# Performance work log

Measured on AMD Instinct MI355X. Metric: run time of the kernel, lower is better.

The kernel has to match this reference:

```python
import jax, jax.numpy as jnp
import numpy as np

N_NODES = 20000
N_EDGES = 200000
N_TOK = 8          # N patch tokens per node
IN_DIM = 64        # C
N_HEADS = 4
HEAD_DIM = 16      # out_dim


def setup_inputs() -> dict:
    key = jax.random.key(0)
    ks = jax.random.split(key, 16)
    scale = 1.0 / np.sqrt(IN_DIM).astype(np.float32)
    def lin(i):
        W = jax.random.normal(ks[i], (IN_DIM, N_HEADS * HEAD_DIM), dtype=jnp.float32) * scale
        b = jax.random.normal(ks[i + 1], (N_HEADS * HEAD_DIM,), dtype=jnp.float32) * 0.01
        return W, b
    Qw, Qb = lin(0)
    Kw, Kb = lin(2)
    Vw, Vb = lin(4)
    Ew, Eb = lin(6)
    h = jax.random.normal(ks[8], (N_NODES, N_TOK, IN_DIM), dtype=jnp.float32)
    e = jax.random.normal(ks[9], (N_EDGES, N_TOK, IN_DIM), dtype=jnp.float32)
    src = jax.random.randint(ks[10], (N_EDGES,), 0, N_NODES)
    dst = jax.random.randint(ks[11], (N_EDGES,), 0, N_NODES)
    return {"h": h, "e": e, "src": src, "dst": dst,
            "Qw": Qw, "Qb": Qb, "Kw": Kw, "Kb": Kb,
            "Vw": Vw, "Vb": Vb, "Ew": Ew, "Eb": Eb}


def _proj(x, W, b):
    # x: [M, N, C] -> [M, N, H, D]
    y = x @ W + b
    return y.reshape(x.shape[0], x.shape[1], N_HEADS, HEAD_DIM)


def reference(h, e, src, dst, Qw, Qb, Kw, Kb, Vw, Vb, Ew, Eb):
    Qh = _proj(h, Qw, Qb)   # [n, N, H, D]
    Kh = _proj(h, Kw, Kb)
    Vh = _proj(h, Vw, Vb)
    pe = _proj(e, Ew, Eb)   # [E, N, H, D]
    inv_sqrt_d = jnp.float32(1.0 / np.sqrt(HEAD_DIM))
    # edge-wise elementwise QK score, scaled, plus relative PE
    score = Kh[src] * Qh[dst] * inv_sqrt_d + pe   # [E, N, H, D]
    e_out = score
    # exp of head-dim-summed clamped score
    s = jnp.exp(jnp.clip(jnp.sum(score, axis=-1, keepdims=True), -5.0, 5.0))  # [E, N, H, 1]
    wV = jax.ops.segment_sum(Vh[src] * s, dst, num_segments=N_NODES)  # [n, N, H, D]
    z = jax.ops.segment_sum(s, dst, num_segments=N_NODES)             # [n, N, H, 1]
    h_out = wV / (z + 1e-6)
    return h_out, e_out
```

## Files before the change

### kernel.cpp

```cpp
#include <hip/hip_runtime.h>
#include <hip/hip_bf16.h>

#define IN_DIM 64
#define N_TOK 8
#define OUT_DIM 64
#define HEAD_DIM 16
#define N_HEADS 4

__global__ void zero_kernel(int* p, int n) {
    int i = blockIdx.x * blockDim.x + threadIdx.x;
    if (i < n) p[i] = 0;
}

__global__ void hist_kernel(const int* __restrict__ dst, int* __restrict__ deg, int n) {
    int i = blockIdx.x * blockDim.x + threadIdx.x;
    if (i < n) atomicAdd(&deg[dst[i]], 1);
}

__global__ void scan_kernel(const int* __restrict__ deg, int* __restrict__ offs,
                            int* __restrict__ cur, int n) {
    __shared__ int wsum[17];
    __shared__ int carry;
    const int tid = threadIdx.x;
    const int lane = tid & 63;
    const int wid = tid >> 6;
    if (tid == 0) carry = 0;
    __syncthreads();
    for (int base = 0; base < n; base += 1024) {
        const int i = base + tid;
        const int v = (i < n) ? deg[i] : 0;
        int x = v;
#pragma unroll
        for (int d = 1; d < 64; d <<= 1) {
            int y = __shfl_up(x, d);
            if (lane >= d) x += y;
        }
        if (lane == 63) wsum[wid] = x;
        __syncthreads();
        if (wid == 0 && lane < 16) {
            const int a = wsum[lane];
            int s = a;
#pragma unroll
            for (int d = 1; d < 16; d <<= 1) {
                int y = __shfl_up(s, d);
                if (lane >= d) s += y;
            }
            wsum[lane] = s - a;
            if (lane == 15) wsum[16] = s;
        }
        __syncthreads();
        const int excl = x - v + wsum[wid] + carry;
        if (i < n) { offs[i] = excl; cur[i] = excl; }
        __syncthreads();
        if (tid == 0) carry += wsum[16];
        __syncthreads();
    }
    if (tid == 0) offs[n] = carry;
}

__global__ void scatter_kernel(const int* __restrict__ dst, int* __restrict__ cur,
                               int* __restrict__ csr, int n) {
    int i = blockIdx.x * blockDim.x + threadIdx.x;
    if (i < n) {
        int pos = atomicAdd(&cur[dst[i]], 1);
        csr[pos] = i;
    }
}

__device__ __forceinline__ void proj16_acc(const float* __restrict__ tile, int lane,
                                           const float* __restrict__ wb,
                                           float acc[16]) {
#pragma unroll 8
    for (int k = 0; k < 64; ++k) {
        const float ev = tile[lane * 65 + k];
        const float4 w0 = *reinterpret_cast<const float4*>(wb + k * 64);
        const float4 w1 = *reinterpret_cast<const float4*>(wb + k * 64 + 4);
        const float4 w2 = *reinterpret_cast<const float4*>(wb + k * 64 + 8);
        const float4 w3 = *reinterpret_cast<const float4*>(wb + k * 64 + 12);
        acc[0]  = fmaf(ev, w0.x, acc[0]);
        acc[1]  = fmaf(ev, w0.y, acc[1]);
        acc[2]  = fmaf(ev, w0.z, acc[2]);
        acc[3]  = fmaf(ev, w0.w, acc[3]);
        acc[4]  = fmaf(ev, w1.x, acc[4]);
        acc[5]  = fmaf(ev, w1.y, acc[5]);
        acc[6]  = fmaf(ev, w1.z, acc[6]);
        acc[7]  = fmaf(ev, w1.w, acc[7]);
        acc[8]  = fmaf(ev, w2.x, acc[8]);
        acc[9]  = fmaf(ev, w2.y, acc[9]);
        acc[10] = fmaf(ev, w2.z, acc[10]);
        acc[11] = fmaf(ev, w2.w, acc[11]);
        acc[12] = fmaf(ev, w3.x, acc[12]);
        acc[13] = fmaf(ev, w3.y, acc[13]);
        acc[14] = fmaf(ev, w3.z, acc[14]);
        acc[15] = fmaf(ev, w3.w, acc[15]);
    }
}

__device__ __forceinline__ void init16_bias(const float* __restrict__ bb, float acc[16]) {
    const float4 b0 = *reinterpret_cast<const float4*>(bb);
    const float4 b1 = *reinterpret_cast<const float4*>(bb + 4);
    const float4 b2 = *reinterpret_cast<const float4*>(bb + 8);
    const float4 b3 = *reinterpret_cast<const float4*>(bb + 12);
    acc[0] = b0.x;  acc[1] = b0.y;  acc[2] = b0.z;  acc[3] = b0.w;
    acc[4] = b1.x;  acc[5] = b1.y;  acc[6] = b1.z;  acc[7] = b1.w;
    acc[8] = b2.x;  acc[9] = b2.y;  acc[10] = b2.z; acc[11] = b2.w;
    acc[12] = b3.x; acc[13] = b3.y; acc[14] = b3.z; acc[15] = b3.w;
}

__global__ void __launch_bounds__(256) hproj_kernel(
    const float* __restrict__ h,
    const float* __restrict__ Qw, const float* __restrict__ Qb,
    const float* __restrict__ Kw, const float* __restrict__ Kb,
    const float* __restrict__ Vw, const float* __restrict__ Vb,
    float* __restrict__ Qh, float* __restrict__ Kh, float* __restrict__ Vh,
    int nrows) {
    __shared__ float tile[64 * 65];
    const int t = threadIdx.x;
    const int lane = t & 63;
    const int chunk = __builtin_amdgcn_readfirstlane(t >> 6);
    const int row0 = blockIdx.x * 64;
    if (row0 >= nrows) return;

#pragma unroll
    for (int i = 0; i < 4; ++i) {
        const int f = i * 1024 + t * 4;
        const float4 v = *reinterpret_cast<const float4*>(h + (size_t)row0 * 64 + f);
        const int r = f >> 6, c = f & 63;
        tile[r * 65 + c + 0] = v.x;
        tile[r * 65 + c + 1] = v.y;
        tile[r * 65 + c + 2] = v.z;
        tile[r * 65 + c + 3] = v.w;
    }
    __syncthreads();

    float aq[16], ak[16], av[16];
    init16_bias(Qb + chunk * 16, aq);
    proj16_acc(tile, lane, Qw + chunk * 16, aq);
    init16_bias(Kb + chunk * 16, ak);
    proj16_acc(tile, lane, Kw + chunk * 16, ak);
    init16_bias(Vb + chunk * 16, av);
    proj16_acc(tile, lane, Vw + chunk * 16, av);

    __syncthreads();
#pragma unroll
    for (int j = 0; j < 16; ++j) tile[lane * 65 + chunk * 16 + j] = aq[j] * 0.25f;
    __syncthreads();
#pragma unroll
    for (int i = 0; i < 4; ++i) {
        const int f = i * 1024 + t * 4;
        const int r = f >> 6, c = f & 63;
        *reinterpret_cast<float4*>(Qh + (size_t)row0 * 64 + f) =
            make_float4(tile[r * 65 + c], tile[r * 65 + c + 1],
                        tile[r * 65 + c + 2], tile[r * 65 + c + 3]);
    }
    __syncthreads();
#pragma unroll
    for (int j = 0; j < 16; ++j) tile[lane * 65 + chunk * 16 + j] = ak[j];
    __syncthreads();
#pragma unroll
    for (int i = 0; i < 4; ++i) {
        const int f = i * 1024 + t * 4;
        const int r = f >> 6, c = f & 63;
        *reinterpret_cast<float4*>(Kh + (size_t)row0 * 64 + f) =
            make_float4(tile[r * 65 + c], tile[r * 65 + c + 1],
                        tile[r * 65 + c + 2], tile[r * 65 + c + 3]);
    }
    __syncthreads();
#pragma unroll
    for (int j = 0; j < 16; ++j) tile[lane * 65 + chunk * 16 + j] = av[j];
    __syncthreads();
#pragma unroll
    for (int i = 0; i < 4; ++i) {
        const int f = i * 1024 + t * 4;
        const int r = f >> 6, c = f & 63;
        *reinterpret_cast<float4*>(Vh + (size_t)row0 * 64 + f) =
            make_float4(tile[r * 65 + c], tile[r * 65 + c + 1],
                        tile[r * 65 + c + 2], tile[r * 65 + c + 3]);
    }
}

__global__ void __launch_bounds__(256) edge_kernel(
    const float* __restrict__ e,
    const int* __restrict__ src, const int* __restrict__ dst,
    const float* __restrict__ Ew, const float* __restrict__ Eb,
    const float* __restrict__ Qh, const float* __restrict__ Kh,
    float* __restrict__ e_out, float* __restrict__ s_buf,
    int npairs, int n_edges) {
    __shared__ float et[64 * 65];
    __shared__ float kt[64 * 68];
    __shared__ float qt[64 * 68];
    const int t = threadIdx.x;
    const int lane = t & 63;
    const int chunk = __builtin_amdgcn_readfirstlane(t >> 6);
    const int p0 = blockIdx.x * 64;
    const int e0 = p0 >> 3;
    if (p0 >= npairs) return;

#pragma unroll
    for (int i = 0; i < 4; ++i) {
        const int f = i * 1024 + t * 4;
        const float4 v = *reinterpret_cast<const float4*>(e + (size_t)p0 * 64 + f);
        const int r = f >> 6, c = f & 63;
        et[r * 65 + c + 0] = v.x;
        et[r * 65 + c + 1] = v.y;
        et[r * 65 + c + 2] = v.z;
        et[r * 65 + c + 3] = v.w;
    }

    float4* kt4 = reinterpret_cast<float4*>(kt);
    float4* qt4 = reinterpret_cast<float4*>(qt);
#pragma unroll
    for (int i = 0; i < 4; ++i) {
        const int f = i * 1024 + t * 4;
        int ee = e0 + (f >> 9);
        if (ee >= n_edges) ee = n_edges - 1;
        const int o = f & 511;
        const int se = src[ee];
        const int de = dst[ee];
        const float4 kv = *reinterpret_cast<const float4*>(Kh + (size_t)se * 512 + o);
        const float4 qv = *reinterpret_cast<const float4*>(Qh + (size_t)de * 512 + o);
        const int r = f >> 6, c4 = (f & 63) >> 2;
        kt4[r * 17 + c4] = kv;
        qt4[r * 17 + c4] = qv;
    }
    __syncthreads();

    float acc[16];
    init16_bias(Eb + chunk * 16, acc);
    proj16_acc(et, lane, Ew + chunk * 16, acc);

#pragma unroll
    for (int c4 = 0; c4 < 4; ++c4) {
        const float4 kv = kt4[lane * 17 + chunk * 4 + c4];
        const float4 qv = qt4[lane * 17 + chunk * 4 + c4];
        acc[c4 * 4 + 0] = fmaf(kv.x, qv.x, acc[c4 * 4 + 0]);
        acc[c4 * 4 + 1] = fmaf(kv.y, qv.y, acc[c4 * 4 + 1]);
        acc[c4 * 4 + 2] = fmaf(kv.z, qv.z, acc[c4 * 4 + 2]);
        acc[c4 * 4 + 3] = fmaf(kv.w, qv.w, acc[c4 * 4 + 3]);
    }

    {
        float s01 = (acc[0] + acc[1]) + (acc[2] + acc[3]);
        float s23 = (acc[4] + acc[5]) + (acc[6] + acc[7]);
        float s45 = (acc[8] + acc[9]) + (acc[10] + acc[11]);
        float s67 = (acc[12] + acc[13]) + (acc[14] + acc[15]);
        float ssum = (s01 + s23) + (s45 + s67);
        ssum = fminf(fmaxf(ssum, -5.f), 5.f);
        s_buf[(size_t)chunk * npairs + p0 + lane] = __expf(ssum);
    }

    __syncthreads();
#pragma unroll
    for (int j = 0; j < 16; ++j) et[lane * 65 + chunk * 16 + j] = acc[j];
    __syncthreads();
#pragma unroll
    for (int i = 0; i < 4; ++i) {
        const int f = i * 1024 + t * 4;
        const int r = f >> 6, c = f & 63;
        *reinterpret_cast<float4*>(e_out + (size_t)p0 * 64 + f) =
            make_float4(et[r * 65 + c], et[r * 65 + c + 1],
                        et[r * 65 + c + 2], et[r * 65 + c + 3]);
    }
}

__global__ void __launch_bounds__(256) gather_kernel(
    const float* __restrict__ Vh, const float* __restrict__ s_buf,
    const int* __restrict__ src,
    const int* __restrict__ offs, const int* __restrict__ csr,
    float* __restrict__ h_out, int nunits, int npairs) {
    const int unit = blockIdx.x * 4 + (threadIdx.x >> 6);
    const int lane = threadIdx.x & 63;
    if (unit >= nunits) return;
    const int node = unit >> 3;
    const int tok = unit & 7;
    const int beg = offs[node];
    const int end = offs[node + 1];
    const int hh = lane >> 4;
    const float* sb = s_buf + (size_t)hh * npairs + tok;
    float acc = 0.f;
    float z = 0.f;
    for (int base = beg; base < end; base += 64) {
        const int nn = min(64, end - base);
        int eid = 0, sidx = 0;
        if (lane < nn) {
            eid = csr[base + lane];
            sidx = src[eid];
        }
        int j = 0;
        for (; j + 1 < nn; j += 2) {
            const int ej0 = __shfl(eid, j),     ej1 = __shfl(eid, j + 1);
            const int sj0 = __shfl(sidx, j),    sj1 = __shfl(sidx, j + 1);
            const float sh0 = sb[(size_t)ej0 * 8];
            const float sh1 = sb[(size_t)ej1 * 8];
            const float v0 = Vh[((size_t)sj0 * 8 + tok) * 64 + lane];
            const float v1 = Vh[((size_t)sj1 * 8 + tok) * 64 + lane];
            acc = fmaf(v0, sh0, acc); z += sh0;
            acc = fmaf(v1, sh1, acc); z += sh1;
        }
        if (j < nn) {
            const int ej = __shfl(eid, j);
            const int sj = __shfl(sidx, j);
            const float sh = sb[(size_t)ej * 8];
            const float v = Vh[((size_t)sj * 8 + tok) * 64 + lane];
            acc = fmaf(v, sh, acc); z += sh;
        }
    }
    h_out[(size_t)unit * OUT_DIM + lane] = acc / (z + 1e-6f);
}

extern "C" void kernel_launch(void* const* d_in, const int* in_sizes, int n_in,
                              void* d_out, int out_size, void* d_ws, size_t ws_size,
                              hipStream_t stream) {
    const float* h  = (const float*)d_in[0];
    const float* e  = (const float*)d_in[1];
    const int* src  = (const int*)d_in[2];
    const int* dst  = (const int*)d_in[3];
    const float* Qw = (const float*)d_in[4];
    const float* Qb = (const float*)d_in[5];
    const float* Kw = (const float*)d_in[6];
    const float* Kb = (const float*)d_in[7];
    const float* Vw = (const float*)d_in[8];
    const float* Vb = (const float*)d_in[9];
    const float* Ew = (const float*)d_in[10];
    const float* Eb = (const float*)d_in[11];

    const int n_nodes = in_sizes[0] / (N_TOK * IN_DIM);
    const int n_edges = in_sizes[2];
    const int nrows   = n_nodes * N_TOK;
    const int npairs  = n_edges * N_TOK;
    const int h_out_elems = n_nodes * N_TOK * OUT_DIM;

    float* h_out = (float*)d_out;
    float* e_out = (float*)d_out + h_out_elems;

    float* Qh    = (float*)d_ws;
    float* Kh    = Qh + (size_t)nrows * OUT_DIM;
    float* Vh    = Kh + (size_t)nrows * OUT_DIM;
    float* s_buf = Vh + (size_t)nrows * OUT_DIM;
    int*   deg   = (int*)(s_buf + (size_t)npairs * N_HEADS);
    int*   offs  = deg + n_nodes;
    int*   cur   = offs + (n_nodes + 1);
    int*   csr   = cur + n_nodes;

    zero_kernel<<<(n_nodes + 255) / 256, 256, 0, stream>>>(deg, n_nodes);
    hist_kernel<<<(n_edges + 255) / 256, 256, 0, stream>>>(dst, deg, n_edges);
    scan_kernel<<<1, 1024, 0, stream>>>(deg, offs, cur, n_nodes);
    scatter_kernel<<<(n_edges + 255) / 256, 256, 0, stream>>>(dst, cur, csr, n_edges);

    hproj_kernel<<<(nrows + 63) / 64, 256, 0, stream>>>(
        h, Qw, Qb, Kw, Kb, Vw, Vb, Qh, Kh, Vh, nrows);

    edge_kernel<<<(npairs + 63) / 64, 256, 0, stream>>>(
        e, src, dst, Ew, Eb, Qh, Kh, e_out, s_buf, npairs, n_edges);

    gather_kernel<<<(nrows + 3) / 4, 256, 0, stream>>>(
        Vh, s_buf, src, offs, csr, h_out, nrows, npairs);
}
```

Measured before the change: 990.4 us.

## Store scores pair-major and gather four tokens per wave with float4 loads

The exp scores buffer is now laid out per pair with the heads contiguous, so one edge's 32 scores sit together. The gather kernel assigns each wavefront four tokens of a node and has each lane handle four output dims via float4 loads and stores. This amortizes the CSR index loads and shuffles across tokens and vectorizes the V gathers. In exchange it launches fewer waves and makes the score writes in the edge kernel strided.

```diff
diff --git a/kernel.cpp b/kernel.cpp
--- a/kernel.cpp
+++ b/kernel.cpp
@@ -246,7 +246,7 @@
         float s67 = (acc[12] + acc[13]) + (acc[14] + acc[15]);
         float ssum = (s01 + s23) + (s45 + s67);
         ssum = fminf(fmaxf(ssum, -5.f), 5.f);
-        s_buf[(size_t)chunk * npairs + p0 + lane] = __expf(ssum);
+        s_buf[(size_t)(p0 + lane) * N_HEADS + chunk] = __expf(ssum);
     }
 
     __syncthreads();
@@ -267,17 +267,18 @@
     const float* __restrict__ Vh, const float* __restrict__ s_buf,
     const int* __restrict__ src,
     const int* __restrict__ offs, const int* __restrict__ csr,
-    float* __restrict__ h_out, int nunits, int npairs) {
-    const int unit = blockIdx.x * 4 + (threadIdx.x >> 6);
+    float* __restrict__ h_out, int n_nodes) {
+    const int gid = blockIdx.x * 4 + (threadIdx.x >> 6);
     const int lane = threadIdx.x & 63;
-    if (unit >= nunits) return;
-    const int node = unit >> 3;
-    const int tok = unit & 7;
+    const int node = gid >> 1;
+    if (node >= n_nodes) return;
+    const int tok = ((gid & 1) << 2) + (lane >> 4);
+    const int dim0 = (lane & 15) << 2;
+    const int soff = (tok << 2) + (dim0 >> 4);
+    const int voff = (tok << 6) + dim0;
     const int beg = offs[node];
     const int end = offs[node + 1];
-    const int hh = lane >> 4;
-    const float* sb = s_buf + (size_t)hh * npairs + tok;
-    float acc = 0.f;
+    float4 acc = make_float4(0.f, 0.f, 0.f, 0.f);
     float z = 0.f;
     for (int base = beg; base < end; base += 64) {
         const int nn = min(64, end - base);
@@ -288,24 +289,41 @@
         }
         int j = 0;
         for (; j + 1 < nn; j += 2) {
-            const int ej0 = __shfl(eid, j),     ej1 = __shfl(eid, j + 1);
-            const int sj0 = __shfl(sidx, j),    sj1 = __shfl(sidx, j + 1);
-            const float sh0 = sb[(size_t)ej0 * 8];
-            const float sh1 = sb[(size_t)ej1 * 8];
-            const float v0 = Vh[((size_t)sj0 * 8 + tok) * 64 + lane];
-            const float v1 = Vh[((size_t)sj1 * 8 + tok) * 64 + lane];
-            acc = fmaf(v0, sh0, acc); z += sh0;
-            acc = fmaf(v1, sh1, acc); z += sh1;
+            const int ej0 = __shfl(eid, j),  ej1 = __shfl(eid, j + 1);
+            const int sj0 = __shfl(sidx, j), sj1 = __shfl(sidx, j + 1);
+            const float sh0 = s_buf[(size_t)ej0 * 32 + soff];
+            const float sh1 = s_buf[(size_t)ej1 * 32 + soff];
+            const float4 v0 = *reinterpret_cast<const float4*>(
+                Vh + (size_t)sj0 * 512 + voff);
+            const float4 v1 = *reinterpret_cast<const float4*>(
+                Vh + (size_t)sj1 * 512 + voff);
+            acc.x = fmaf(v0.x, sh0, acc.x);
+            acc.y = fmaf(v0.y, sh0, acc.y);
+            acc.z = fmaf(v0.z, sh0, acc.z);
+            acc.w = fmaf(v0.w, sh0, acc.w);
+            z += sh0;
+            acc.x = fmaf(v1.x, sh1, acc.x);
+            acc.y = fmaf(v1.y, sh1, acc.y);
+            acc.z = fmaf(v1.z, sh1, acc.z);
+            acc.w = fmaf(v1.w, sh1, acc.w);
+            z += sh1;
         }
         if (j < nn) {
             const int ej = __shfl(eid, j);
             const int sj = __shfl(sidx, j);
-            const float sh = sb[(size_t)ej * 8];
-            const float v = Vh[((size_t)sj * 8 + tok) * 64 + lane];
-            acc = fmaf(v, sh, acc); z += sh;
-        }
-    }
-    h_out[(size_t)unit * OUT_DIM + lane] = acc / (z + 1e-6f);
+            const float sh = s_buf[(size_t)ej * 32 + soff];
+            const float4 v = *reinterpret_cast<const float4*>(
+                Vh + (size_t)sj * 512 + voff);
+            acc.x = fmaf(v.x, sh, acc.x);
+            acc.y = fmaf(v.y, sh, acc.y);
+            acc.z = fmaf(v.z, sh, acc.z);
+            acc.w = fmaf(v.w, sh, acc.w);
+            z += sh;
+        }
+    }
+    const float inv = 1.f / (z + 1e-6f);
+    *reinterpret_cast<float4*>(h_out + ((size_t)node * 8 + tok) * 64 + dim0) =
+        make_float4(acc.x * inv, acc.y * inv, acc.z * inv, acc.w * inv);
 }
 
 extern "C" void kernel_launch(void* const* d_in, const int* in_sizes, int n_in,
@@ -353,6 +371,6 @@
     edge_kernel<<<(npairs + 63) / 64, 256, 0, stream>>>(
         e, src, dst, Ew, Eb, Qh, Kh, e_out, s_buf, npairs, n_edges);
 
-    gather_kernel<<<(nrows + 3) / 4, 256, 0, stream>>>(
-        Vh, s_buf, src, offs, csr, h_out, nrows, npairs);
-}
+    gather_kernel<<<(n_nodes * 2 + 3) / 4, 256, 0, stream>>>(
+        Vh, s_buf, src, offs, csr, h_out, n_nodes);
+}
```

After: 954.3 us. 3.6% less time.
